# Performance work log

Measured on AMD Instinct MI355X. Metric: run time of the kernel, lower is better.

## Reference

```python
import jax, jax.numpy as jnp
import numpy as np

EPS = 1e-8

def _penalty(v, lo, hi):
    # if v<lo: (lo-v)/lo ; elif v>hi (hi finite): (v-hi)/hi ; else 0
    below = (lo - v) / lo
    if np.isinf(hi):
        return jnp.where(v < lo, below, 0.0)
    above = (v - hi) / hi
    return jnp.where(v < lo, below, jnp.where(v > hi, above, 0.0))

def _symbolic_features(x):
    # x: [B, input_dim]; column mapping from the original per-row loop
    am, bod, do, ph, nit = x[:, 0], x[:, 1], x[:, 2], x[:, 4], x[:, 7]
    # penalties in param_order = [ph, ammonia, bod, dissolved_oxygen, nitrate]
    p_ph  = _penalty(ph, 6.5, 8.5)
    p_am  = _penalty(am, 0.001, 0.5)
    p_bod = _penalty(bod, 0.001, 5.0)
    p_do  = _penalty(do, 6.0, np.inf)
    p_nit = _penalty(nit, 0.001, 10.0)
    # pollutant scores (missing params like 'nitrogen'/'orthophosphate' are skipped -> count adjusts)
    s_bact = (1.2 * am / (0.5 + EPS) + 1.5 * bod / (5.0 + EPS) - 0.8 * do / (10.0 + EPS)) / 3.0
    s_chem = (1.5 * ph / (8.5 + EPS) + 1.0 * nit / (10.0 + EPS)) / 2.0
    s_org  = (2.0 * bod / (5.0 + EPS) - 1.5 * do / (10.0 + EPS) + 0.8 * am / (0.5 + EPS)) / 3.0
    s_agr  = (2.0 * nit / (10.0 + EPS)) / 1.0
    resil = 1.0 / (1.0 + (p_ph + p_am + p_bod + p_do + p_nit) + EPS)
    return jnp.stack([p_ph, p_am, p_bod, p_do, p_nit, s_bact, s_chem, s_org, s_agr, resil], axis=1)

def setup_inputs() -> dict:
    key = jax.random.key(0)
    ks = jax.random.split(key, 16)
    B, D_IN, SYM, H = 1048576, 10, 10, 64
    def lin(k, fin, fout):
        k1, k2 = jax.random.split(k)
        s = 1.0 / np.sqrt(fin)
        return (jax.random.uniform(k1, (fin, fout), jnp.float32, -s, s),
                jax.random.uniform(k2, (fout,), jnp.float32, -s, s))
    W_sym, b_sym = lin(ks[0], SYM, H // 2)
    W_in, b_in = lin(ks[1], D_IN + H // 2, H)
    W1, b1 = lin(ks[2], H, H)
    W2, b2 = lin(ks[3], H, H)
    W3, b3 = lin(ks[4], H, H)
    W_r1, b_r1 = lin(ks[5], H, H // 2)
    W_r2, b_r2 = lin(ks[6], H // 2, 1)
    W_c1, b_c1 = lin(ks[7], H, H // 2)
    W_c2, b_c2 = lin(ks[8], H // 2, 4)
    x = jax.random.uniform(ks[9], (B, D_IN), jnp.float32)
    return {"x": x, "W_sym": W_sym, "b_sym": b_sym, "W_in": W_in, "b_in": b_in,
            "W1": W1, "b1": b1, "W2": W2, "b2": b2, "W3": W3, "b3": b3,
            "W_r1": W_r1, "b_r1": b_r1, "W_r2": W_r2, "b_r2": b_r2,
            "W_c1": W_c1, "b_c1": b_c1, "W_c2": W_c2, "b_c2": b_c2}

def reference(x, W_sym, b_sym, W_in, b_in, W1, b1, W2, b2, W3, b3,
              W_r1, b_r1, W_r2, b_r2, W_c1, b_c1, W_c2, b_c2):
    elu = jax.nn.elu
    sym = _symbolic_features(x)                      # [B, 10]
    sym_enc = elu(sym @ W_sym + b_sym)               # [B, 32]  (Dropout: eval mode = identity)
    h = elu(jnp.concatenate([x, sym_enc], axis=1) @ W_in + b_in)  # [B, 64]
    for W, b in ((W1, b1), (W2, b2), (W3, b3)):
        h = h + elu(h @ W + b)                       # residual MLP stack
    predictions = elu(h @ W_r1 + b_r1) @ W_r2 + b_r2            # [B, 1]
    pollutant_logits = elu(h @ W_c1 + b_c1) @ W_c2 + b_c2       # [B, 4]
    return predictions, pollutant_logits
```

## Files before the change

kernel.cpp:

```cpp
#include <hip/hip_runtime.h>
#include <hip/hip_bf16.h>
#include <math.h>

#define NROWS 1048576
#define EPSF 1e-8f
#define GRID 2048
#define TPB 256
#define ITERS 4

typedef unsigned short ushortT;
typedef __attribute__((ext_vector_type(8))) short short8;
typedef __attribute__((ext_vector_type(4))) short short4v;
typedef __attribute__((ext_vector_type(4))) float floatx4;
typedef __attribute__((ext_vector_type(2))) int int2v;

#define WS_HI   256
#define WS_LO   41216
#define WS_MF   82176
#define MF_B5   0
#define MF_WSYM 320
#define MF_BSYM 640
#define MF_WR2  672
#define MF_BR2  704
#define MF_WC2  708
#define MF_BC2  836
#define MF_WC2T 840
#define MF_TOTAL 968

#define LDS_FENCE() asm volatile("s_waitcnt lgkmcnt(0)" ::: "memory")

struct WPtrs { const void* p[19]; };

__device__ __forceinline__ float ldw(const void* p, int i, bool f32) {
    return f32 ? ((const float*)p)[i]
               : __uint_as_float(((unsigned)((const ushortT*)p)[i]) << 16);
}

__device__ __forceinline__ int sniff_f32(const void* x) {
    const ushortT v = ((const ushortT*)x)[threadIdx.x & 63];
    const unsigned long long m = __ballot((v & 0x8000u) != 0);
    return (m != 0ull) ? 1 : 0;
}

__global__ void prep_kernel(WPtrs wp, void* __restrict__ ws) {
    __shared__ int flagS;
    if (threadIdx.x < 64) {
        const int f = sniff_f32(wp.p[0]);
        if (threadIdx.x == 0) flagS = f;
    }
    __syncthreads();
    const bool f32 = (flagS != 0);

    ushortT* hi = (ushortT*)((char*)ws + WS_HI);
    ushortT* lo = (ushortT*)((char*)ws + WS_LO);
    float* mf = (float*)((char*)ws + WS_MF);
    const int B = blockIdx.x;
    if (B < 5) {
        const int L = B;
        for (int idx = threadIdx.x; idx < 4096; idx += 256) {
            const int j8 = idx & 7, ln = (idx >> 3) & 63, s2 = (idx >> 9) & 1, t = idx >> 10;
            const int s = 2 * s2 + (j8 >> 2), j = j8 & 3;
            const int k = 16 * s + 4 * (ln >> 4) + j;
            const int m = 16 * t + (ln & 15);
            float w = 0.0f;
            if (L == 0)      { if (k < 42) w = ldw(wp.p[3], k * 64 + m, f32); }
            else if (L <= 3) { if (k < 64) w = ldw(wp.p[3 + 2 * L], k * 64 + m, f32); }
            else             { if (k < 64) w = (m < 32) ? ldw(wp.p[11], k * 32 + m, f32)
                                                        : ldw(wp.p[15], k * 32 + (m - 32), f32); }
            const unsigned u = __float_as_uint(w);
            const float rem = w - __uint_as_float(u & 0xffff0000u);
            hi[L * 4096 + idx] = (ushortT)(u >> 16);
            lo[L * 4096 + idx] = (ushortT)(__float_as_uint(rem) >> 16);
        }
    } else {
        const int src[12] = {4, 6, 8, 10, 12, 16, 1, 2, 13, 14, 17, 18};
        const int cnt[12] = {64, 64, 64, 64, 32, 32, 320, 32, 32, 1, 128, 4};
        const int dst[12] = {0, 64, 128, 192, 256, 288, MF_WSYM, MF_BSYM, MF_WR2, MF_BR2, MF_WC2, MF_BC2};
        for (int a = 0; a < 12; ++a)
            for (int i = threadIdx.x; i < cnt[a]; i += 256)
                mf[dst[a] + i] = ldw(wp.p[src[a]], i, f32);
        for (int i = threadIdx.x; i < 128; i += 256) {
            const int qq = i >> 5, j = i & 31;
            mf[MF_WC2T + i] = ldw(wp.p[17], j * 4 + qq, f32);
        }
    }
}

__device__ __forceinline__ float eluf(float v) {
    return fmaxf(v, 0.0f) + (__expf(fminf(v, 0.0f)) - 1.0f);
}

__device__ __forceinline__ unsigned pack_hi16(unsigned ua, unsigned ub) {
    return __builtin_amdgcn_perm(ub, ua, 0x07060302u);
}

__device__ __forceinline__ void split4(float a0, float a1, float a2, float a3,
                                       short4v& h4, short4v& l4) {
    const unsigned u0 = __float_as_uint(a0), u1 = __float_as_uint(a1);
    const unsigned u2 = __float_as_uint(a2), u3 = __float_as_uint(a3);
    int2v h, l;
    h[0] = (int)pack_hi16(u0, u1);
    h[1] = (int)pack_hi16(u2, u3);
    const float l0 = a0 - __uint_as_float(u0 & 0xffff0000u);
    const float l1 = a1 - __uint_as_float(u1 & 0xffff0000u);
    const float l2 = a2 - __uint_as_float(u2 & 0xffff0000u);
    const float l3 = a3 - __uint_as_float(u3 & 0xffff0000u);
    l[0] = (int)pack_hi16(__float_as_uint(l0), __float_as_uint(l1));
    l[1] = (int)pack_hi16(__float_as_uint(l2), __float_as_uint(l3));
    h4 = __builtin_bit_cast(short4v, h);
    l4 = __builtin_bit_cast(short4v, l);
}

__device__ __forceinline__ void put4(short8& d, int hh, short4v s) {
    d[4 * hh + 0] = s[0]; d[4 * hh + 1] = s[1];
    d[4 * hh + 2] = s[2]; d[4 * hh + 3] = s[3];
}

__device__ __forceinline__ floatx4 mfma32(short8 a, short8 b, floatx4 c) {
#if __has_builtin(__builtin_amdgcn_mfma_f32_16x16x32_bf16)
    return __builtin_amdgcn_mfma_f32_16x16x32_bf16(a, b, c, 0, 0, 0);
#else
    const short4v ae = {a[0], a[1], a[2], a[3]}, ao = {a[4], a[5], a[6], a[7]};
    const short4v be = {b[0], b[1], b[2], b[3]}, bo = {b[4], b[5], b[6], b[7]};
    c = __builtin_amdgcn_mfma_f32_16x16x16bf16_1k(ae, be, c, 0, 0, 0);
    c = __builtin_amdgcn_mfma_f32_16x16x16bf16_1k(ao, bo, c, 0, 0, 0);
    return c;
#endif
}

template<bool F32>
__device__ __forceinline__ void run_body(
    const void* __restrict__ xin, const char* __restrict__ wsb,
    void* __restrict__ out,
    const float* __restrict__ mflds,
    float (* __restrict__ hb)[68],
    const int lane, const int wavebase)
{
    const short8* __restrict__ Ahi = (const short8*)(wsb + WS_HI) + lane;
    const short8* __restrict__ Alo = (const short8*)(wsb + WS_LO) + lane;
    const int n = lane & 15, q = lane >> 4;

    #pragma unroll
    for (int i = 0; i < 6; ++i) {
        const int c = 42 + q * 6 + i;
        if (c < 64) hb[n][c] = 0.0f;
    }

    unsigned xu[2][5];
    float xf[2][10];
    #pragma unroll
    for (int u = 0; u < 2; ++u) {
        const int rowg = wavebase + 16 * u + n;
        if (F32) {
            const float* xp = (const float*)xin + (size_t)rowg * 10;
            #pragma unroll
            for (int i = 0; i < 10; ++i) xf[u][i] = xp[i];
        } else {
            const unsigned* xd = (const unsigned*)((const ushortT*)xin + (size_t)rowg * 10);
            #pragma unroll
            for (int i = 0; i < 5; ++i) xu[u][i] = xd[i];
        }
    }

    #pragma unroll 1
    for (int it = 0; it < ITERS; ++it) {
        const int rowbase = wavebase + it * 32;
        short8 Bhi8[2][2], Blo8[2][2];

        #pragma unroll
        for (int u = 0; u < 2; ++u) {
            float x[10];
            if (F32) {
                #pragma unroll
                for (int i = 0; i < 10; ++i) x[i] = xf[u][i];
            } else {
                #pragma unroll
                for (int i = 0; i < 5; ++i) {
                    const unsigned d = xu[u][i];
                    x[2 * i]     = __uint_as_float(d << 16);
                    x[2 * i + 1] = __uint_as_float(d & 0xffff0000u);
                }
            }
            if (q == 0) {
                #pragma unroll
                for (int i = 0; i < 10; ++i) hb[n][i] = x[i];
            }

            const float am = x[0], bod = x[1], dox = x[2], ph = x[4], nit = x[7];
            const float p_ph  = ph  < 6.5f   ? (6.5f - ph) * 0.15384616f
                              : (ph > 8.5f   ? (ph - 8.5f) * 0.11764706f : 0.0f);
            const float p_am  = am  < 0.001f ? (0.001f - am) * 1000.0f
                              : (am > 0.5f   ? (am - 0.5f) * 2.0f : 0.0f);
            const float p_bod = bod < 0.001f ? (0.001f - bod) * 1000.0f
                              : (bod > 5.0f  ? (bod - 5.0f) * 0.2f : 0.0f);
            const float p_do  = dox < 6.0f   ? (6.0f - dox) * 0.16666667f : 0.0f;
            const float p_nit = nit < 0.001f ? (0.001f - nit) * 1000.0f
                              : (nit > 10.0f ? (nit - 10.0f) * 0.1f : 0.0f);
            const float s_bact = (am * 2.3999999f + bod * 0.29999998f - dox * 0.08f) * 0.33333334f;
            const float s_chem = (ph * 0.17647059f + nit * 0.1f) * 0.5f;
            const float s_org  = (bod * 0.39999998f - dox * 0.14999999f + am * 1.5999999f) * 0.33333334f;
            const float s_agr  = nit * 0.2f;
            const float resil  = 1.0f / (1.0f + (p_ph + p_am + p_bod + p_do + p_nit) + EPSF);
            const float sym[10] = {p_ph, p_am, p_bod, p_do, p_nit, s_bact, s_chem, s_org, s_agr, resil};

            float se[8];
            {
                const floatx4 b0 = *(const floatx4*)(mflds + MF_BSYM + q * 8);
                const floatx4 b1 = *(const floatx4*)(mflds + MF_BSYM + q * 8 + 4);
                #pragma unroll
                for (int jj = 0; jj < 4; ++jj) { se[jj] = b0[jj]; se[4 + jj] = b1[jj]; }
                #pragma unroll
                for (int k = 0; k < 10; ++k) {
                    const floatx4 w0 = *(const floatx4*)(mflds + MF_WSYM + k * 32 + q * 8);
                    const floatx4 w1 = *(const floatx4*)(mflds + MF_WSYM + k * 32 + q * 8 + 4);
                    #pragma unroll
                    for (int jj = 0; jj < 4; ++jj) {
                        se[jj]     = fmaf(sym[k], w0[jj], se[jj]);
                        se[4 + jj] = fmaf(sym[k], w1[jj], se[4 + jj]);
                    }
                }
            }
            #pragma unroll
            for (int jj = 0; jj < 8; ++jj) hb[n][10 + q * 8 + jj] = eluf(se[jj]);
            LDS_FENCE();
            #pragma unroll
            for (int s2 = 0; s2 < 2; ++s2) {
                #pragma unroll
                for (int hh = 0; hh < 2; ++hh) {
                    const floatx4 v = *(const floatx4*)&hb[n][16 * (2 * s2 + hh) + 4 * q];
                    short4v h4, l4;
                    split4(v[0], v[1], v[2], v[3], h4, l4);
                    put4(Bhi8[u][s2], hh, h4);
                    put4(Blo8[u][s2], hh, l4);
                }
            }
            LDS_FENCE();
        }

        {
            const int itn = (it + 1 < ITERS) ? it + 1 : it;
            #pragma unroll
            for (int u = 0; u < 2; ++u) {
                const int rowg = wavebase + itn * 32 + 16 * u + n;
                if (F32) {
                    const float* xp = (const float*)xin + (size_t)rowg * 10;
                    #pragma unroll
                    for (int i = 0; i < 10; ++i) xf[u][i] = xp[i];
                } else {
                    const unsigned* xd = (const unsigned*)((const ushortT*)xin + (size_t)rowg * 10);
                    #pragma unroll
                    for (int i = 0; i < 5; ++i) xu[u][i] = xd[i];
                }
            }
        }

        float hprev[2][4][4];
        #pragma unroll
        for (int L = 0; L < 5; ++L) {
            short8 Ap[8];
            #pragma unroll
            for (int c = 0; c < 8; ++c) Ap[c] = Ahi[L * 512 + c * 64];
            short8 Alp[8];
            if (F32) {
                #pragma unroll
                for (int c = 0; c < 8; ++c) Alp[c] = Alo[L * 512 + c * 64];
            }

            floatx4 acc[2][4];
            #pragma unroll
            for (int t = 0; t < 4; ++t) {
                const floatx4 b = *(const floatx4*)(mflds + MF_B5 + L * 64 + 16 * t + 4 * q);
                acc[0][t] = b; acc[1][t] = b;
            }
            #pragma unroll
            for (int t = 0; t < 4; ++t) {
                #pragma unroll
                for (int s2 = 0; s2 < 2; ++s2) {
                    const short8 A = Ap[2 * t + s2];
                    #pragma unroll
                    for (int u = 0; u < 2; ++u) {
                        acc[u][t] = mfma32(A, Bhi8[u][s2], acc[u][t]);
                        acc[u][t] = mfma32(A, Blo8[u][s2], acc[u][t]);
                    }
                    if (F32) {
                        const short8 Al = Alp[2 * t + s2];
                        #pragma unroll
                        for (int u = 0; u < 2; ++u)
                            acc[u][t] = mfma32(Al, Bhi8[u][s2], acc[u][t]);
                    }
                }
            }

            if (L < 4) {
                #pragma unroll
                for (int u = 0; u < 2; ++u) {
                    #pragma unroll
                    for (int t = 0; t < 4; ++t) {
                        #pragma unroll
                        for (int r = 0; r < 4; ++r) {
                            float e = eluf(acc[u][t][r]);
                            if (L >= 1) e += hprev[u][t][r];
                            hprev[u][t][r] = e;
                        }
                        short4v h4, l4;
                        split4(hprev[u][t][0], hprev[u][t][1],
                               hprev[u][t][2], hprev[u][t][3], h4, l4);
                        put4(Bhi8[u][t >> 1], t & 1, h4);
                        put4(Blo8[u][t >> 1], t & 1, l4);
                    }
                }
            } else {
                const floatx4 wr0 = *(const floatx4*)(mflds + MF_WR2 + 4 * q);
                const floatx4 wr1 = *(const floatx4*)(mflds + MF_WR2 + 16 + 4 * q);
                #pragma unroll
                for (int u = 0; u < 2; ++u) {
                    float pred = (q == 0) ? mflds[MF_BR2] : 0.0f;
                    float z2[4], z3[4];
                    #pragma unroll
                    for (int r = 0; r < 4; ++r) {
                        pred = fmaf(eluf(acc[u][0][r]), wr0[r], pred);
                        pred = fmaf(eluf(acc[u][1][r]), wr1[r], pred);
                        z2[r] = eluf(acc[u][2][r]);
                        z3[r] = eluf(acc[u][3][r]);
                    }
                    float lg[4];
                    #pragma unroll
                    for (int c = 0; c < 4; ++c) {
                        const floatx4 wc0 = *(const floatx4*)(mflds + MF_WC2T + c * 32 + 4 * q);
                        const floatx4 wc1 = *(const floatx4*)(mflds + MF_WC2T + c * 32 + 16 + 4 * q);
                        float l = (q == 0) ? mflds[MF_BC2 + c] : 0.0f;
                        #pragma unroll
                        for (int r = 0; r < 4; ++r) {
                            l = fmaf(z2[r], wc0[r], l);
                            l = fmaf(z3[r], wc1[r], l);
                        }
                        lg[c] = l;
                    }
                    pred += __shfl_xor(pred, 16, 64);
                    pred += __shfl_xor(pred, 32, 64);
                    #pragma unroll
                    for (int c = 0; c < 4; ++c) {
                        lg[c] += __shfl_xor(lg[c], 16, 64);
                        lg[c] += __shfl_xor(lg[c], 32, 64);
                    }
                    const float lsel = q == 0 ? lg[0] : (q == 1 ? lg[1] : (q == 2 ? lg[2] : lg[3]));
                    const int rowg = rowbase + 16 * u + n;
                    if (F32) {
                        float* o = (float*)out;
                        if (q == 0) o[rowg] = pred;
                        o[NROWS + rowg * 4 + q] = lsel;
                    } else {
                        __hip_bfloat16* o = (__hip_bfloat16*)out;
                        if (q == 0) o[rowg] = __float2bfloat16(pred);
                        o[NROWS + rowg * 4 + q] = __float2bfloat16(lsel);
                    }
                }
            }
        }
    }
}

__device__ __forceinline__ int kernel_prologue(const void* xin, const void* ws,
                                               float* mflds, int* flagS) {
    const int tid = threadIdx.x;
    if (tid < 64) {
        const int f = sniff_f32(xin);
        if (tid == 0) *flagS = f;
    }
    {
        const float* mfsrc = (const float*)((const char*)ws + WS_MF);
        for (int i = tid; i < MF_TOTAL; i += TPB) mflds[i] = mfsrc[i];
    }
    __syncthreads();
    return *flagS;
}

__global__ __launch_bounds__(TPB, 3) void mlp_bf16_kernel(
    const void* __restrict__ xin, const void* __restrict__ ws, void* __restrict__ out)
{
    __shared__ __align__(16) float mflds[MF_TOTAL];
    __shared__ float hball[4][16][68];
    __shared__ int flagS;
    if (kernel_prologue(xin, ws, mflds, &flagS) != 0) return;
    const int tid = threadIdx.x;
    const int wave = tid >> 6, lane = tid & 63;
    const int gw = blockIdx.x * 4 + wave;
    const int wavebase = gw * (32 * ITERS);
    run_body<false>(xin, (const char*)ws, out, mflds, hball[wave], lane, wavebase);
}

__global__ __launch_bounds__(TPB, 2) void mlp_f32_kernel(
    const void* __restrict__ xin, const void* __restrict__ ws, void* __restrict__ out)
{
    __shared__ __align__(16) float mflds[MF_TOTAL];
    __shared__ float hball[4][16][68];
    __shared__ int flagS;
    if (kernel_prologue(xin, ws, mflds, &flagS) == 0) return;
    const int tid = threadIdx.x;
    const int wave = tid >> 6, lane = tid & 63;
    const int gw = blockIdx.x * 4 + wave;
    const int wavebase = gw * (32 * ITERS);
    run_body<true>(xin, (const char*)ws, out, mflds, hball[wave], lane, wavebase);
}

extern "C" void kernel_launch(void* const* d_in, const int* in_sizes, int n_in,
                              void* d_out, int out_size, void* d_ws, size_t ws_size,
                              hipStream_t stream) {
    (void)in_sizes; (void)n_in; (void)out_size; (void)ws_size;

    WPtrs wp;
    for (int i = 0; i < 19; ++i) wp.p[i] = d_in[i];
    prep_kernel<<<6, 256, 0, stream>>>(wp, d_ws);

    mlp_bf16_kernel<<<GRID, TPB, 0, stream>>>(d_in[0], d_ws, d_out);
    mlp_f32_kernel<<<GRID, TPB, 0, stream>>>(d_in[0], d_ws, d_out);
}
```

Baseline: 359.2 us.

## Compute symbolic encoder with MFMA, async-load x to LDS, stream W_lo loads

Replaces the scalar 10x32 symbolic-encoder FMA loop with split-precision bf16 MFMA using a new pre-packed W_sym fragment, and rearranges the input layer's K ordering so x and the encoder output feed the B fragments directly. For the f32 path, x rows are double-buffered into LDS with global_load_lds, and the low-precision weight fragments are loaded two at a time instead of all eight up front. The f32 kernel's occupancy bound rises from 2 to 3 blocks, and it now launches before the bf16 kernel. This trades LDS traffic and extra fences for fewer VALU ops and registers, with some risk to the hi/lo split accuracy and LDS layout correctness.

```diff
diff --git a/kernel.cpp b/kernel.cpp
--- a/kernel.cpp
+++ b/kernel.cpp
@@ -12,11 +12,14 @@
 typedef __attribute__((ext_vector_type(8))) short short8;
 typedef __attribute__((ext_vector_type(4))) short short4v;
 typedef __attribute__((ext_vector_type(4))) float floatx4;
+typedef __attribute__((ext_vector_type(2))) float floatx2;
 typedef __attribute__((ext_vector_type(2))) int int2v;
 
 #define WS_HI   256
 #define WS_LO   41216
 #define WS_MF   82176
+#define WS_SYH  86272
+#define WS_SYL  87296
 #define MF_B5   0
 #define MF_WSYM 320
 #define MF_BSYM 640
@@ -27,7 +30,10 @@
 #define MF_WC2T 840
 #define MF_TOTAL 968
 
+#define ENCP 44
+
 #define LDS_FENCE() asm volatile("s_waitcnt lgkmcnt(0)" ::: "memory")
+#define VM_FENCE()  asm volatile("s_waitcnt vmcnt(0)" ::: "memory")
 
 struct WPtrs { const void* p[19]; };
 
@@ -41,6 +47,26 @@
     const unsigned long long m = __ballot((v & 0x8000u) != 0);
     return (m != 0ull) ? 1 : 0;
 }
+
+#if __has_builtin(__builtin_amdgcn_global_load_lds)
+typedef __attribute__((address_space(1))) const void gas_void;
+typedef __attribute__((address_space(3))) void las_void;
+__device__ __forceinline__ void gl_lds16(const void* g, void* l) {
+    __builtin_amdgcn_global_load_lds((gas_void*)g, (las_void*)l, 16, 0, 0);
+}
+__device__ __forceinline__ void gl_lds4(const void* g, void* l) {
+    __builtin_amdgcn_global_load_lds((gas_void*)g, (las_void*)l, 4, 0, 0);
+}
+#else
+__device__ __forceinline__ void gl_lds16(const void* g, void* l) {
+    const int lane = threadIdx.x & 63;
+    ((floatx4*)l)[lane] = ((const floatx4*)g)[lane];
+}
+__device__ __forceinline__ void gl_lds4(const void* g, void* l) {
+    const int lane = threadIdx.x & 63;
+    ((float*)l)[lane] = ((const float*)g)[lane];
+}
+#endif
 
 __global__ void prep_kernel(WPtrs wp, void* __restrict__ ws) {
     __shared__ int flagS;
@@ -63,7 +89,10 @@
             const int k = 16 * s + 4 * (ln >> 4) + j;
             const int m = 16 * t + (ln & 15);
             float w = 0.0f;
-            if (L == 0)      { if (k < 42) w = ldw(wp.p[3], k * 64 + m, f32); }
+            if (L == 0) {
+                if (k < 10)                 w = ldw(wp.p[3], k * 64 + m, f32);
+                else if (k >= 12 && k < 44) w = ldw(wp.p[3], (k - 2) * 64 + m, f32);
+            }
             else if (L <= 3) { if (k < 64) w = ldw(wp.p[3 + 2 * L], k * 64 + m, f32); }
             else             { if (k < 64) w = (m < 32) ? ldw(wp.p[11], k * 32 + m, f32)
                                                         : ldw(wp.p[15], k * 32 + (m - 32), f32); }
@@ -82,6 +111,19 @@
         for (int i = threadIdx.x; i < 128; i += 256) {
             const int qq = i >> 5, j = i & 31;
             mf[MF_WC2T + i] = ldw(wp.p[17], j * 4 + qq, f32);
+        }
+        ushortT* syh = (ushortT*)((char*)ws + WS_SYH);
+        ushortT* syl = (ushortT*)((char*)ws + WS_SYL);
+        for (int idx = threadIdx.x; idx < 512; idx += 256) {
+            const int j = idx & 3, ln = (idx >> 2) & 63, t = idx >> 8;
+            const int k = 4 * (ln >> 4) + j;
+            const int m = 16 * t + (ln & 15);
+            float w = 0.0f;
+            if (k < 10) w = ldw(wp.p[1], k * 32 + m, f32);
+            const unsigned u = __float_as_uint(w);
+            const float rem = w - __uint_as_float(u & 0xffff0000u);
+            syh[idx] = (ushortT)(u >> 16);
+            syl[idx] = (ushortT)(__float_as_uint(rem) >> 16);
         }
     }
 }
@@ -127,52 +169,81 @@
     return c;
 #endif
 }
+__device__ __forceinline__ floatx4 mfma16(short4v a, short4v b, floatx4 c) {
+#if __has_builtin(__builtin_amdgcn_mfma_f32_16x16x16bf16_1k)
+    return __builtin_amdgcn_mfma_f32_16x16x16bf16_1k(a, b, c, 0, 0, 0);
+#else
+    const short8 a8 = {a[0], a[1], a[2], a[3], 0, 0, 0, 0};
+    const short8 b8 = {b[0], b[1], b[2], b[3], 0, 0, 0, 0};
+    return mfma32(a8, b8, c);
+#endif
+}
 
 template<bool F32>
 __device__ __forceinline__ void run_body(
     const void* __restrict__ xin, const char* __restrict__ wsb,
     void* __restrict__ out,
     const float* __restrict__ mflds,
-    float (* __restrict__ hb)[68],
+    float* __restrict__ hb,
+    float* __restrict__ xbuf,
     const int lane, const int wavebase)
 {
     const short8* __restrict__ Ahi = (const short8*)(wsb + WS_HI) + lane;
     const short8* __restrict__ Alo = (const short8*)(wsb + WS_LO) + lane;
+    const short4v* __restrict__ Syh = (const short4v*)(wsb + WS_SYH) + lane;
+    const short4v* __restrict__ Syl = (const short4v*)(wsb + WS_SYL) + lane;
     const int n = lane & 15, q = lane >> 4;
 
     #pragma unroll
-    for (int i = 0; i < 6; ++i) {
-        const int c = 42 + q * 6 + i;
-        if (c < 64) hb[n][c] = 0.0f;
-    }
-
-    unsigned xu[2][5];
-    float xf[2][10];
-    #pragma unroll
-    for (int u = 0; u < 2; ++u) {
-        const int rowg = wavebase + 16 * u + n;
-        if (F32) {
-            const float* xp = (const float*)xin + (size_t)rowg * 10;
-            #pragma unroll
-            for (int i = 0; i < 10; ++i) xf[u][i] = xp[i];
-        } else {
-            const unsigned* xd = (const unsigned*)((const ushortT*)xin + (size_t)rowg * 10);
-            #pragma unroll
-            for (int i = 0; i < 5; ++i) xu[u][i] = xd[i];
-        }
+    for (int i = 0; i < 4; ++i) {
+        const int id = lane * 4 + i;
+        hb[(id >> 7) * (16 * ENCP) + ((id >> 3) & 15) * ENCP + 32 + (id & 7)] = 0.0f;
+    }
+
+    if (F32) {
+        const float* g = (const float*)xin + (size_t)wavebase * 10;
+        gl_lds16(g + lane * 4, xbuf);
+        gl_lds4(g + 256 + lane, xbuf + 256);
     }
 
     #pragma unroll 1
     for (int it = 0; it < ITERS; ++it) {
         const int rowbase = wavebase + it * 32;
+        const int cur = it & 1;
+
+        if (F32) {
+            VM_FENCE();
+            const int itn = (it + 1 < ITERS) ? it + 1 : it;
+            const float* g = (const float*)xin + (size_t)(wavebase + itn * 32) * 10;
+            float* xb = xbuf + (cur ^ 1) * 320;
+            gl_lds16(g + lane * 4, xb);
+            gl_lds4(g + 256 + lane, xb + 256);
+        }
+        unsigned xu[2][5];
+        if (!F32) {
+            #pragma unroll
+            for (int u = 0; u < 2; ++u) {
+                const unsigned* xd = (const unsigned*)((const ushortT*)xin
+                                     + (size_t)(rowbase + 16 * u + n) * 10);
+                #pragma unroll
+                for (int i = 0; i < 5; ++i) xu[u][i] = xd[i];
+            }
+        }
+
         short8 Bhi8[2][2], Blo8[2][2];
+        const short4v As0 = Syh[0], As1 = Syh[64];
+        const short4v Az0 = Syl[0], Az1 = Syl[64];
 
         #pragma unroll
         for (int u = 0; u < 2; ++u) {
             float x[10];
             if (F32) {
-                #pragma unroll
-                for (int i = 0; i < 10; ++i) x[i] = xf[u][i];
+                const float* xr = xbuf + cur * 320 + (16 * u + n) * 10;
+                #pragma unroll
+                for (int i = 0; i < 5; ++i) {
+                    const floatx2 v = *(const floatx2*)(xr + 2 * i);
+                    x[2 * i] = v[0]; x[2 * i + 1] = v[1];
+                }
             } else {
                 #pragma unroll
                 for (int i = 0; i < 5; ++i) {
@@ -180,10 +251,6 @@
                     x[2 * i]     = __uint_as_float(d << 16);
                     x[2 * i + 1] = __uint_as_float(d & 0xffff0000u);
                 }
-            }
-            if (q == 0) {
-                #pragma unroll
-                for (int i = 0; i < 10; ++i) hb[n][i] = x[i];
             }
 
             const float am = x[0], bod = x[1], dox = x[2], ph = x[4], nit = x[7];
@@ -203,55 +270,43 @@
             const float resil  = 1.0f / (1.0f + (p_ph + p_am + p_bod + p_do + p_nit) + EPSF);
             const float sym[10] = {p_ph, p_am, p_bod, p_do, p_nit, s_bact, s_chem, s_org, s_agr, resil};
 
-            float se[8];
-            {
-                const floatx4 b0 = *(const floatx4*)(mflds + MF_BSYM + q * 8);
-                const floatx4 b1 = *(const floatx4*)(mflds + MF_BSYM + q * 8 + 4);
-                #pragma unroll
-                for (int jj = 0; jj < 4; ++jj) { se[jj] = b0[jj]; se[4 + jj] = b1[jj]; }
-                #pragma unroll
-                for (int k = 0; k < 10; ++k) {
-                    const floatx4 w0 = *(const floatx4*)(mflds + MF_WSYM + k * 32 + q * 8);
-                    const floatx4 w1 = *(const floatx4*)(mflds + MF_WSYM + k * 32 + q * 8 + 4);
-                    #pragma unroll
-                    for (int jj = 0; jj < 4; ++jj) {
-                        se[jj]     = fmaf(sym[k], w0[jj], se[jj]);
-                        se[4 + jj] = fmaf(sym[k], w1[jj], se[4 + jj]);
-                    }
-                }
-            }
+            const float b0 = q == 0 ? sym[0] : q == 1 ? sym[4] : q == 2 ? sym[8] : 0.0f;
+            const float b1 = q == 0 ? sym[1] : q == 1 ? sym[5] : q == 2 ? sym[9] : 0.0f;
+            const float b2 = q == 0 ? sym[2] : q == 1 ? sym[6] : 0.0f;
+            const float b3 = q == 0 ? sym[3] : q == 1 ? sym[7] : 0.0f;
+            short4v bh, bl;
+            split4(b0, b1, b2, b3, bh, bl);
+            floatx4 sa0 = *(const floatx4*)(mflds + MF_BSYM + 4 * q);
+            floatx4 sa1 = *(const floatx4*)(mflds + MF_BSYM + 16 + 4 * q);
+            sa0 = mfma16(As0, bh, sa0); sa0 = mfma16(As0, bl, sa0); sa0 = mfma16(Az0, bh, sa0);
+            sa1 = mfma16(As1, bh, sa1); sa1 = mfma16(As1, bl, sa1); sa1 = mfma16(Az1, bh, sa1);
+
+            float* hrow = hb + u * (16 * ENCP) + n * ENCP;
+            floatx4 e0, e1;
             #pragma unroll
-            for (int jj = 0; jj < 8; ++jj) hb[n][10 + q * 8 + jj] = eluf(se[jj]);
+            for (int r = 0; r < 4; ++r) { e0[r] = eluf(sa0[r]); e1[r] = eluf(sa1[r]); }
+            *(floatx4*)(hrow + 4 * q) = e0;
+            *(floatx4*)(hrow + 16 + 4 * q) = e1;
             LDS_FENCE();
-            #pragma unroll
-            for (int s2 = 0; s2 < 2; ++s2) {
-                #pragma unroll
-                for (int hh = 0; hh < 2; ++hh) {
-                    const floatx4 v = *(const floatx4*)&hb[n][16 * (2 * s2 + hh) + 4 * q];
-                    short4v h4, l4;
-                    split4(v[0], v[1], v[2], v[3], h4, l4);
-                    put4(Bhi8[u][s2], hh, h4);
-                    put4(Blo8[u][s2], hh, l4);
-                }
-            }
-            LDS_FENCE();
-        }
-
-        {
-            const int itn = (it + 1 < ITERS) ? it + 1 : it;
-            #pragma unroll
-            for (int u = 0; u < 2; ++u) {
-                const int rowg = wavebase + itn * 32 + 16 * u + n;
-                if (F32) {
-                    const float* xp = (const float*)xin + (size_t)rowg * 10;
-                    #pragma unroll
-                    for (int i = 0; i < 10; ++i) xf[u][i] = xp[i];
-                } else {
-                    const unsigned* xd = (const unsigned*)((const ushortT*)xin + (size_t)rowg * 10);
-                    #pragma unroll
-                    for (int i = 0; i < 5; ++i) xu[u][i] = xd[i];
-                }
-            }
+
+            const floatx4 enc03 = *(const floatx4*)(hrow + 0);
+            const floatx4 f1 = *(const floatx4*)(hrow + 4 + 4 * q);
+            const floatx4 f2 = *(const floatx4*)(hrow + 20 + 4 * q);
+            const float a0 = q == 0 ? x[0] : q == 1 ? x[4] : x[8];
+            const float a1 = q == 0 ? x[1] : q == 1 ? x[5] : x[9];
+            const float a2 = q == 0 ? x[2] : q == 1 ? x[6] : 0.0f;
+            const float a3 = q == 0 ? x[3] : q == 1 ? x[7] : 0.0f;
+            const floatx4 f0 = { q == 3 ? enc03[0] : a0, q == 3 ? enc03[1] : a1,
+                                 q == 3 ? enc03[2] : a2, q == 3 ? enc03[3] : a3 };
+            short4v h4, l4;
+            split4(f0[0], f0[1], f0[2], f0[3], h4, l4);
+            put4(Bhi8[u][0], 0, h4); put4(Blo8[u][0], 0, l4);
+            split4(f1[0], f1[1], f1[2], f1[3], h4, l4);
+            put4(Bhi8[u][0], 1, h4); put4(Blo8[u][0], 1, l4);
+            split4(f2[0], f2[1], f2[2], f2[3], h4, l4);
+            put4(Bhi8[u][1], 0, h4); put4(Blo8[u][1], 0, l4);
+            const short4v z4 = {0, 0, 0, 0};
+            put4(Bhi8[u][1], 1, z4); put4(Blo8[u][1], 1, z4);
         }
 
         float hprev[2][4][4];
@@ -260,11 +315,8 @@
             short8 Ap[8];
             #pragma unroll
             for (int c = 0; c < 8; ++c) Ap[c] = Ahi[L * 512 + c * 64];
-            short8 Alp[8];
-            if (F32) {
-                #pragma unroll
-                for (int c = 0; c < 8; ++c) Alp[c] = Alo[L * 512 + c * 64];
-            }
+            short8 AlpA, AlpB;
+            if (F32) { AlpA = Alo[L * 512]; AlpB = Alo[L * 512 + 64]; }
 
             floatx4 acc[2][4];
             #pragma unroll
@@ -274,6 +326,11 @@
             }
             #pragma unroll
             for (int t = 0; t < 4; ++t) {
+                const short8 Al0 = AlpA, Al1 = AlpB;
+                if (F32 && t < 3) {
+                    AlpA = Alo[L * 512 + (2 * t + 2) * 64];
+                    AlpB = Alo[L * 512 + (2 * t + 3) * 64];
+                }
                 #pragma unroll
                 for (int s2 = 0; s2 < 2; ++s2) {
                     const short8 A = Ap[2 * t + s2];
@@ -283,7 +340,7 @@
                         acc[u][t] = mfma32(A, Blo8[u][s2], acc[u][t]);
                     }
                     if (F32) {
-                        const short8 Al = Alp[2 * t + s2];
+                        const short8 Al = s2 ? Al1 : Al0;
                         #pragma unroll
                         for (int u = 0; u < 2; ++u)
                             acc[u][t] = mfma32(Al, Bhi8[u][s2], acc[u][t]);
@@ -375,32 +432,35 @@
     return *flagS;
 }
 
+__global__ __launch_bounds__(TPB, 3) void mlp_f32_kernel(
+    const void* __restrict__ xin, const void* __restrict__ ws, void* __restrict__ out)
+{
+    __shared__ __align__(16) float mflds[MF_TOTAL];
+    __shared__ __align__(16) float hball[4][2][16][ENCP];
+    __shared__ __align__(16) float xball[4][2][320];
+    __shared__ int flagS;
+    if (kernel_prologue(xin, ws, mflds, &flagS) == 0) return;
+    const int tid = threadIdx.x;
+    const int wave = tid >> 6, lane = tid & 63;
+    const int gw = blockIdx.x * 4 + wave;
+    const int wavebase = gw * (32 * ITERS);
+    run_body<true>(xin, (const char*)ws, out, mflds,
+                   &hball[wave][0][0][0], &xball[wave][0][0], lane, wavebase);
+}
+
 __global__ __launch_bounds__(TPB, 3) void mlp_bf16_kernel(
     const void* __restrict__ xin, const void* __restrict__ ws, void* __restrict__ out)
 {
     __shared__ __align__(16) float mflds[MF_TOTAL];
-    __shared__ float hball[4][16][68];
+    __shared__ __align__(16) float hball[4][2][16][ENCP];
     __shared__ int flagS;
     if (kernel_prologue(xin, ws, mflds, &flagS) != 0) return;
     const int tid = threadIdx.x;
     const int wave = tid >> 6, lane = tid & 63;
     const int gw = blockIdx.x * 4 + wave;
     const int wavebase = gw * (32 * ITERS);
-    run_body<false>(xin, (const char*)ws, out, mflds, hball[wave], lane, wavebase);
-}
-
-__global__ __launch_bounds__(TPB, 2) void mlp_f32_kernel(
-    const void* __restrict__ xin, const void* __restrict__ ws, void* __restrict__ out)
-{
-    __shared__ __align__(16) float mflds[MF_TOTAL];
-    __shared__ float hball[4][16][68];
-    __shared__ int flagS;
-    if (kernel_prologue(xin, ws, mflds, &flagS) == 0) return;
-    const int tid = threadIdx.x;
-    const int wave = tid >> 6, lane = tid & 63;
-    const int gw = blockIdx.x * 4 + wave;
-    const int wavebase = gw * (32 * ITERS);
-    run_body<true>(xin, (const char*)ws, out, mflds, hball[wave], lane, wavebase);
+    run_body<false>(xin, (const char*)ws, out, mflds,
+                    &hball[wave][0][0][0], nullptr, lane, wavebase);
 }
 
 extern "C" void kernel_launch(void* const* d_in, const int* in_sizes, int n_in,
@@ -412,6 +472,6 @@
     for (int i = 0; i < 19; ++i) wp.p[i] = d_in[i];
     prep_kernel<<<6, 256, 0, stream>>>(wp, d_ws);
 
+    mlp_f32_kernel<<<GRID, TPB, 0, stream>>>(d_in[0], d_ws, d_out);
     mlp_bf16_kernel<<<GRID, TPB, 0, stream>>>(d_in[0], d_ws, d_out);
-    mlp_f32_kernel<<<GRID, TPB, 0, stream>>>(d_in[0], d_ws, d_out);
-}
+}
```

Result: slower. 599.1 us (+66.8%).
